# Kernel optimization log

Hardware: AMD Instinct MI355X
Metric: run time of the kernel (lower is better)

Reference implementation:

```python
import jax, jax.numpy as jnp
import numpy as np

N, DIN, DOUT = 8192, 128, 128
NEG = -9.0e15  # the module's -9000000000000000.0 mask value
ALPHA = 0.2    # LeakyReLU negative slope


def setup_inputs() -> dict:
    key = jax.random.key(0)
    kx, ka, kw, ks, kr = jax.random.split(key, 5)
    X = jax.random.normal(kx, (N, DIN), dtype=jnp.float32)
    A = (jax.random.uniform(ka, (N, N)) < 0.01).astype(jnp.float32)
    A = A.at[jnp.arange(N), jnp.arange(N)].set(1.0)
    # Linear weight (Kaiming-uniform-ish range is irrelevant to math; use Xavier)
    lim_w = float(np.sqrt(6.0 / (DIN + DOUT)))
    W = jax.random.uniform(kw, (DOUT, DIN), jnp.float32, -lim_w, lim_w)
    b = jnp.zeros((DOUT,), jnp.float32)
    lim_a = float(np.sqrt(6.0 / (DOUT + 1)))
    a_s = jax.random.uniform(ks, (DOUT, 1), jnp.float32, -lim_a, lim_a)
    a_r = jax.random.uniform(kr, (DOUT, 1), jnp.float32, -lim_a, lim_a)
    return {"X": X, "A": A, "W": W, "b": b, "a_s": a_s, "a_r": a_r}


def reference(X, A, W, b, a_s, a_r):
    # H_in = Linear(X)
    H = X @ W.T + b                         # [N, DOUT]
    s = H @ a_s                             # [N, 1] source scores
    r = H @ a_r                             # [N, 1] receiver scores
    # M_s = A * s (broadcast over cols), M_r = A * r^T (broadcast over rows)
    e = jax.nn.leaky_relu(A * s + A * r.T, negative_slope=ALPHA)  # [N, N]
    masked = jnp.where(A > 0, e, NEG)
    att = jax.nn.softmax(masked, axis=1)    # row-stochastic attention
    H_out = att @ H                         # [N, DOUT]  (act = Identity, dropout = eval)
    # NOTE: the torch module applies LayerNorm into a local var but returns
    # the pre-norm H_out, so LayerNorm is dead code. A and [] passthroughs omitted.
    return H_out
```

## Files before the change

### kernel.cpp

```cpp
#include <hip/hip_runtime.h>

#define N 8192
#define D 128
#define ALPHA 0.2f
#define CAP 1536

__global__ __launch_bounds__(256) void linear_kernel(
    const float* __restrict__ X, const float* __restrict__ W,
    const float* __restrict__ b, const float* __restrict__ a_s,
    const float* __restrict__ a_r,
    float* __restrict__ H, float* __restrict__ sv, float* __restrict__ rv)
{
    __shared__ float Xs[128 * 36];
    __shared__ float Ws[64 * 132];

    const int tid = threadIdx.x;
    const int i0  = blockIdx.x * 32;

    for (int idx = tid; idx < 32 * 128; idx += 256) {
        const int row = idx >> 7, k = idx & 127;
        Xs[k * 36 + row] = X[(i0 + row) * D + k];
    }

    float acc[4][4] = {};
    const int ty = tid >> 5, tx = tid & 31;
    const int rbase = ty * 4, cbase = tx * 4;

    for (int kb = 0; kb < 2; ++kb) {
        __syncthreads();
        for (int idx = tid; idx < 64 * 128; idx += 256) {
            const int o = idx >> 6, kk = idx & 63;
            Ws[kk * 132 + o] = W[o * D + kb * 64 + kk];
        }
        __syncthreads();
        #pragma unroll
        for (int kk = 0; kk < 64; ++kk) {
            const float4 xv = *(const float4*)&Xs[(kb * 64 + kk) * 36 + rbase];
            const float4 wv = *(const float4*)&Ws[kk * 132 + cbase];
            const float xr[4] = {xv.x, xv.y, xv.z, xv.w};
            const float wc[4] = {wv.x, wv.y, wv.z, wv.w};
            #pragma unroll
            for (int r = 0; r < 4; ++r)
                #pragma unroll
                for (int c = 0; c < 4; ++c)
                    acc[r][c] += xr[r] * wc[c];
        }
    }

    const float4 bv  = *(const float4*)&b[cbase];
    const float4 asv = *(const float4*)&a_s[cbase];
    const float4 arv = *(const float4*)&a_r[cbase];
    #pragma unroll
    for (int r = 0; r < 4; ++r) {
        float4 h;
        h.x = acc[r][0] + bv.x;
        h.y = acc[r][1] + bv.y;
        h.z = acc[r][2] + bv.z;
        h.w = acc[r][3] + bv.w;
        *(float4*)&H[(size_t)(i0 + rbase + r) * D + cbase] = h;
        float ps = h.x * asv.x + h.y * asv.y + h.z * asv.z + h.w * asv.w;
        float pr = h.x * arv.x + h.y * arv.y + h.z * arv.z + h.w * arv.w;
        #pragma unroll
        for (int off = 16; off > 0; off >>= 1) {
            ps += __shfl_xor(ps, off);
            pr += __shfl_xor(pr, off);
        }
        if (tx == 0) {
            sv[i0 + rbase + r] = ps;
            rv[i0 + rbase + r] = pr;
        }
    }
}

__global__ __launch_bounds__(256) void attn_kernel(
    const float* __restrict__ A, const float* __restrict__ H,
    const float* __restrict__ sv, const float* __restrict__ rv,
    float* __restrict__ out)
{
    __shared__ int   s_idx[CAP];
    __shared__ float s_z[CAP];
    __shared__ int   s_cnt;
    __shared__ float s_redm[4];
    __shared__ float s_reds[4];
    __shared__ float s_hbuf[128];

    const int tid = threadIdx.x;
    const int i   = blockIdx.x;
    if (tid == 0) s_cnt = 0;
    __syncthreads();

    const float  si   = sv[i];
    const float4* Arow = (const float4*)(A + (size_t)i * N);

    float lm = -3.0e38f;
    #pragma unroll
    for (int it = 0; it < 8; ++it) {
        const int idx4 = it * 256 + tid;
        const float4 a = Arow[idx4];
        const float av[4] = {a.x, a.y, a.z, a.w};
        #pragma unroll
        for (int e = 0; e < 4; ++e) {
            if (av[e] != 0.0f) {
                const int j = idx4 * 4 + e;
                float z = si + rv[j];
                z = (z > 0.0f) ? z : ALPHA * z;
                const int p = atomicAdd(&s_cnt, 1);
                if (p < CAP) { s_idx[p] = j; s_z[p] = z; }
                lm = fmaxf(lm, z);
            }
        }
    }

    #pragma unroll
    for (int off = 32; off > 0; off >>= 1) lm = fmaxf(lm, __shfl_xor(lm, off));
    if ((tid & 63) == 0) s_redm[tid >> 6] = lm;
    __syncthreads();
    const int   cnt = (s_cnt < CAP) ? s_cnt : CAP;
    const float m   = fmaxf(fmaxf(s_redm[0], s_redm[1]), fmaxf(s_redm[2], s_redm[3]));

    float sl = 0.0f;
    for (int p = tid; p < cnt; p += 256) {
        const float w = __expf(s_z[p] - m);
        s_z[p] = w;
        sl += w;
    }
    #pragma unroll
    for (int off = 32; off > 0; off >>= 1) sl += __shfl_xor(sl, off);
    if ((tid & 63) == 0) s_reds[tid >> 6] = sl;
    __syncthreads();
    const float inv = 1.0f / (s_reds[0] + s_reds[1] + s_reds[2] + s_reds[3]);

    const int d = tid & 127, half = tid >> 7;
    float acc = 0.0f;
    for (int p = half; p < cnt; p += 2)
        acc += s_z[p] * H[(size_t)s_idx[p] * D + d];

    if (half == 1) s_hbuf[d] = acc;
    __syncthreads();
    if (half == 0) out[(size_t)i * D + d] = (acc + s_hbuf[d]) * inv;
}

extern "C" void kernel_launch(void* const* d_in, const int* in_sizes, int n_in,
                              void* d_out, int out_size, void* d_ws, size_t ws_size,
                              hipStream_t stream) {
    const float* X   = (const float*)d_in[0];
    const float* A   = (const float*)d_in[1];
    const float* W   = (const float*)d_in[2];
    const float* b   = (const float*)d_in[3];
    const float* a_s = (const float*)d_in[4];
    const float* a_r = (const float*)d_in[5];
    float* out = (float*)d_out;

    float* H  = (float*)d_ws;
    float* sv = H + (size_t)N * D;
    float* rv = sv + N;

    linear_kernel<<<256, 256, 0, stream>>>(X, W, b, a_s, a_r, H, sv, rv);
    attn_kernel<<<N, 256, 0, stream>>>(A, H, sv, rv, out);
}
```

Measured before the change: 445.7 us.

## Split attention into global sparse-list scan and wave-per-row gather kernels

Replaces the per-row block that scanned A with shared-memory atomics by a grid-stride scan kernel. That kernel builds per-row neighbor lists in global memory using wave ballots and aggregated atomics. A separate gather kernel then handles each row with one wave, computing the softmax in registers and accumulating H rows as float2. The aim is better memory-level parallelism on the dense A read and cheaper aggregation, at the cost of an extra memset and launch, a per-row cap of 256 neighbors, and a nondeterministic neighbor order.

```diff
diff --git a/kernel.cpp b/kernel.cpp
--- a/kernel.cpp
+++ b/kernel.cpp
@@ -3,7 +3,7 @@
 #define N 8192
 #define D 128
 #define ALPHA 0.2f
-#define CAP 1536
+#define RCAP 256
 
 __global__ __launch_bounds__(256) void linear_kernel(
     const float* __restrict__ X, const float* __restrict__ W,
@@ -72,72 +72,102 @@
     }
 }
 
-__global__ __launch_bounds__(256) void attn_kernel(
-    const float* __restrict__ A, const float* __restrict__ H,
-    const float* __restrict__ sv, const float* __restrict__ rv,
-    float* __restrict__ out)
+__global__ __launch_bounds__(256) void scan_kernel(
+    const float* __restrict__ A, int* __restrict__ cnt, int* __restrict__ lists)
 {
-    __shared__ int   s_idx[CAP];
-    __shared__ float s_z[CAP];
-    __shared__ int   s_cnt;
-    __shared__ float s_redm[4];
-    __shared__ float s_reds[4];
-    __shared__ float s_hbuf[128];
+    const int lane = threadIdx.x & 63;
+    const unsigned long long lt_mask = (lane == 63) ? 0xFFFFFFFFFFFFFFFFull >> 1
+                                                    : (1ull << lane) - 1;
+    int idx = blockIdx.x * 256 + threadIdx.x;
+    const int stride = gridDim.x * 256;
+    const float4* __restrict__ A4 = (const float4*)A;
 
-    const int tid = threadIdx.x;
-    const int i   = blockIdx.x;
-    if (tid == 0) s_cnt = 0;
-    __syncthreads();
+    #pragma unroll 1
+    for (int it = 0; it < 32; ++it, idx += stride) {
+        const float4 a = A4[idx];
+        const int row  = idx >> 11;
+        const int col0 = (idx & 2047) * 4;
+        const float av[4] = {a.x, a.y, a.z, a.w};
+        #pragma unroll
+        for (int e = 0; e < 4; ++e) {
+            const bool nz = (av[e] != 0.0f);
+            const unsigned long long mask = __ballot(nz);
+            if (mask == 0ull) continue;
+            const int leader = __ffsll((long long)mask) - 1;
+            int base = 0;
+            if (lane == leader) base = atomicAdd(&cnt[row], __popcll(mask));
+            base = __shfl(base, leader);
+            if (nz) {
+                const int off = __popcll(mask & lt_mask);
+                const int p = base + off;
+                if (p < RCAP) lists[row * RCAP + p] = col0 + e;
+            }
+        }
+    }
+}
 
-    const float  si   = sv[i];
-    const float4* Arow = (const float4*)(A + (size_t)i * N);
+__global__ __launch_bounds__(256) void gather_kernel(
+    const float* __restrict__ H, const float* __restrict__ sv,
+    const float* __restrict__ rv, const int* __restrict__ cnt,
+    const int* __restrict__ lists, float* __restrict__ out)
+{
+    __shared__ float s_w[4][RCAP];
+    __shared__ int   s_j[4][RCAP];
+
+    const int wave = threadIdx.x >> 6;
+    const int lane = threadIdx.x & 63;
+    const int i = blockIdx.x * 4 + wave;
+
+    int c = cnt[i];
+    c = (c < RCAP) ? c : RCAP;
+    const float si = sv[i];
+
+    float zv[4];
+    int   jv[4];
+    int kn = 0;
+    for (int p = lane; p < c; p += 64, ++kn) {
+        const int j = lists[i * RCAP + p];
+        float z = si + rv[j];
+        z = (z > 0.0f) ? z : ALPHA * z;
+        jv[kn] = j;
+        zv[kn] = z;
+    }
 
     float lm = -3.0e38f;
     #pragma unroll
-    for (int it = 0; it < 8; ++it) {
-        const int idx4 = it * 256 + tid;
-        const float4 a = Arow[idx4];
-        const float av[4] = {a.x, a.y, a.z, a.w};
-        #pragma unroll
-        for (int e = 0; e < 4; ++e) {
-            if (av[e] != 0.0f) {
-                const int j = idx4 * 4 + e;
-                float z = si + rv[j];
-                z = (z > 0.0f) ? z : ALPHA * z;
-                const int p = atomicAdd(&s_cnt, 1);
-                if (p < CAP) { s_idx[p] = j; s_z[p] = z; }
-                lm = fmaxf(lm, z);
-            }
+    for (int k = 0; k < 4; ++k) if (k < kn) lm = fmaxf(lm, zv[k]);
+    #pragma unroll
+    for (int off = 32; off > 0; off >>= 1) lm = fmaxf(lm, __shfl_xor(lm, off));
+
+    float sl = 0.0f;
+    #pragma unroll
+    for (int k = 0; k < 4; ++k) if (k < kn) { zv[k] = __expf(zv[k] - lm); sl += zv[k]; }
+    #pragma unroll
+    for (int off = 32; off > 0; off >>= 1) sl += __shfl_xor(sl, off);
+    const float inv = 1.0f / sl;
+
+    {
+        int k = 0;
+        for (int p = lane; p < c; p += 64, ++k) {
+            s_w[wave][p] = zv[k];
+            s_j[wave][p] = jv[k];
         }
     }
+    __syncthreads();
 
-    #pragma unroll
-    for (int off = 32; off > 0; off >>= 1) lm = fmaxf(lm, __shfl_xor(lm, off));
-    if ((tid & 63) == 0) s_redm[tid >> 6] = lm;
-    __syncthreads();
-    const int   cnt = (s_cnt < CAP) ? s_cnt : CAP;
-    const float m   = fmaxf(fmaxf(s_redm[0], s_redm[1]), fmaxf(s_redm[2], s_redm[3]));
-
-    float sl = 0.0f;
-    for (int p = tid; p < cnt; p += 256) {
-        const float w = __expf(s_z[p] - m);
-        s_z[p] = w;
-        sl += w;
+    float2 acc = make_float2(0.0f, 0.0f);
+    const float* __restrict__ Hl = H + 2 * lane;
+    #pragma unroll 4
+    for (int p = 0; p < c; ++p) {
+        const float w = s_w[wave][p];
+        const int   j = s_j[wave][p];
+        const float2 h = *(const float2*)&Hl[(size_t)j * D];
+        acc.x += w * h.x;
+        acc.y += w * h.y;
     }
-    #pragma unroll
-    for (int off = 32; off > 0; off >>= 1) sl += __shfl_xor(sl, off);
-    if ((tid & 63) == 0) s_reds[tid >> 6] = sl;
-    __syncthreads();
-    const float inv = 1.0f / (s_reds[0] + s_reds[1] + s_reds[2] + s_reds[3]);
-
-    const int d = tid & 127, half = tid >> 7;
-    float acc = 0.0f;
-    for (int p = half; p < cnt; p += 2)
-        acc += s_z[p] * H[(size_t)s_idx[p] * D + d];
-
-    if (half == 1) s_hbuf[d] = acc;
-    __syncthreads();
-    if (half == 0) out[(size_t)i * D + d] = (acc + s_hbuf[d]) * inv;
+    acc.x *= inv;
+    acc.y *= inv;
+    *(float2*)&out[(size_t)i * D + 2 * lane] = acc;
 }
 
 extern "C" void kernel_launch(void* const* d_in, const int* in_sizes, int n_in,
@@ -151,10 +181,14 @@
     const float* a_r = (const float*)d_in[5];
     float* out = (float*)d_out;
 
-    float* H  = (float*)d_ws;
-    float* sv = H + (size_t)N * D;
-    float* rv = sv + N;
+    float* H   = (float*)d_ws;
+    float* sv  = H + (size_t)N * D;
+    float* rv  = sv + N;
+    int*   cnt = (int*)(rv + N);
+    int*   lists = cnt + N;
 
+    hipMemsetAsync(cnt, 0, N * sizeof(int), stream);
     linear_kernel<<<256, 256, 0, stream>>>(X, W, b, a_s, a_r, H, sv, rv);
-    attn_kernel<<<N, 256, 0, stream>>>(A, H, sv, rv, out);
+    scan_kernel<<<2048, 256, 0, stream>>>(A, cnt, lists);
+    gather_kernel<<<2048, 256, 0, stream>>>(H, sv, rv, cnt, lists, out);
 }
```

Result: no change. 452.9 us (+1.6%).

## Process one attention row per wavefront with ballot-based neighbor compaction

Applied to the files above, without the earlier changes.

The attention kernel now assigns one row per 64-lane wavefront (four rows per block), so it no longer needs block-wide barriers or shared-memory reductions. Nonzero columns are compacted with ballot/popcount prefix sums instead of shared atomics, and the loads of A are software-prefetched one step ahead. Softmax runs in registers, and aggregation has each lane accumulate two output columns through float2 loads of H. The risk is the neighbor cap, now 256 per row (about 82 expected per row), which silently truncates unusually dense rows. There is also less memory-level parallelism per row while streaming A.

```diff
diff --git a/kernel.cpp b/kernel.cpp
--- a/kernel.cpp
+++ b/kernel.cpp
@@ -3,7 +3,7 @@
 #define N 8192
 #define D 128
 #define ALPHA 0.2f
-#define CAP 1536
+#define RCAP 256
 
 __global__ __launch_bounds__(256) void linear_kernel(
     const float* __restrict__ X, const float* __restrict__ W,
@@ -72,72 +72,87 @@
     }
 }
 
-__global__ __launch_bounds__(256) void attn_kernel(
+__global__ __launch_bounds__(256, 8) void attn_fused(
     const float* __restrict__ A, const float* __restrict__ H,
     const float* __restrict__ sv, const float* __restrict__ rv,
     float* __restrict__ out)
 {
-    __shared__ int   s_idx[CAP];
-    __shared__ float s_z[CAP];
-    __shared__ int   s_cnt;
-    __shared__ float s_redm[4];
-    __shared__ float s_reds[4];
-    __shared__ float s_hbuf[128];
+    __shared__ float2 s_l[4][RCAP];
 
-    const int tid = threadIdx.x;
-    const int i   = blockIdx.x;
-    if (tid == 0) s_cnt = 0;
-    __syncthreads();
+    const int wave = threadIdx.x >> 6;
+    const int lane = threadIdx.x & 63;
+    const int i    = blockIdx.x * 4 + wave;
+    const unsigned long long lt = (1ull << lane) - 1ull;
 
-    const float  si   = sv[i];
-    const float4* Arow = (const float4*)(A + (size_t)i * N);
+    const float4* __restrict__ Arow = (const float4*)(A + (size_t)i * N);
 
-    float lm = -3.0e38f;
-    #pragma unroll
-    for (int it = 0; it < 8; ++it) {
-        const int idx4 = it * 256 + tid;
-        const float4 a = Arow[idx4];
-        const float av[4] = {a.x, a.y, a.z, a.w};
+    int cnt = 0;
+    float4 cur = Arow[lane];
+    #pragma unroll 1
+    for (int it = 0; it < 32; ++it) {
+        float4 nxt = make_float4(0.f, 0.f, 0.f, 0.f);
+        if (it < 31) nxt = Arow[(it + 1) * 64 + lane];
+        const int col0 = it * 256 + lane * 4;
+        const float av[4] = {cur.x, cur.y, cur.z, cur.w};
         #pragma unroll
         for (int e = 0; e < 4; ++e) {
-            if (av[e] != 0.0f) {
-                const int j = idx4 * 4 + e;
-                float z = si + rv[j];
-                z = (z > 0.0f) ? z : ALPHA * z;
-                const int p = atomicAdd(&s_cnt, 1);
-                if (p < CAP) { s_idx[p] = j; s_z[p] = z; }
-                lm = fmaxf(lm, z);
+            const bool nz = (av[e] != 0.0f);
+            const unsigned long long m = __ballot(nz);
+            if (nz) {
+                const int pos = cnt + __popcll(m & lt);
+                if (pos < RCAP) s_l[wave][pos].y = __int_as_float(col0 + e);
             }
+            cnt += __popcll(m);
         }
+        cur = nxt;
     }
+    cnt = (cnt < RCAP) ? cnt : RCAP;
 
+    const float si = sv[i];
+    float zv[4];
+    #pragma unroll
+    for (int k = 0; k < 4; ++k) {
+        const int p = lane + 64 * k;
+        const bool act = (p < cnt);
+        const int j = act ? __float_as_int(s_l[wave][p].y) : 0;
+        float z = si + rv[j];
+        z = (z > 0.0f) ? z : ALPHA * z;
+        zv[k] = act ? z : -3.0e38f;
+    }
+    float lm = fmaxf(fmaxf(zv[0], zv[1]), fmaxf(zv[2], zv[3]));
     #pragma unroll
     for (int off = 32; off > 0; off >>= 1) lm = fmaxf(lm, __shfl_xor(lm, off));
-    if ((tid & 63) == 0) s_redm[tid >> 6] = lm;
-    __syncthreads();
-    const int   cnt = (s_cnt < CAP) ? s_cnt : CAP;
-    const float m   = fmaxf(fmaxf(s_redm[0], s_redm[1]), fmaxf(s_redm[2], s_redm[3]));
 
     float sl = 0.0f;
-    for (int p = tid; p < cnt; p += 256) {
-        const float w = __expf(s_z[p] - m);
-        s_z[p] = w;
+    float wv4[4];
+    #pragma unroll
+    for (int k = 0; k < 4; ++k) {
+        const int p = lane + 64 * k;
+        const float w = (p < cnt) ? __expf(zv[k] - lm) : 0.0f;
+        wv4[k] = w;
         sl += w;
     }
     #pragma unroll
     for (int off = 32; off > 0; off >>= 1) sl += __shfl_xor(sl, off);
-    if ((tid & 63) == 0) s_reds[tid >> 6] = sl;
-    __syncthreads();
-    const float inv = 1.0f / (s_reds[0] + s_reds[1] + s_reds[2] + s_reds[3]);
+    const float inv = 1.0f / sl;
 
-    const int d = tid & 127, half = tid >> 7;
-    float acc = 0.0f;
-    for (int p = half; p < cnt; p += 2)
-        acc += s_z[p] * H[(size_t)s_idx[p] * D + d];
+    #pragma unroll
+    for (int k = 0; k < 4; ++k) {
+        const int p = lane + 64 * k;
+        if (p < cnt) s_l[wave][p].x = wv4[k] * inv;
+    }
 
-    if (half == 1) s_hbuf[d] = acc;
-    __syncthreads();
-    if (half == 0) out[(size_t)i * D + d] = (acc + s_hbuf[d]) * inv;
+    float2 acc = make_float2(0.0f, 0.0f);
+    const float* __restrict__ Hl = H + 2 * lane;
+    #pragma unroll 4
+    for (int p = 0; p < cnt; ++p) {
+        const float2 wj = s_l[wave][p];
+        const int   j  = __float_as_int(wj.y);
+        const float2 h = *(const float2*)&Hl[(size_t)j * D];
+        acc.x += wj.x * h.x;
+        acc.y += wj.x * h.y;
+    }
+    *(float2*)&out[(size_t)i * D + 2 * lane] = acc;
 }
 
 extern "C" void kernel_launch(void* const* d_in, const int* in_sizes, int n_in,
@@ -156,5 +171,5 @@
     float* rv = sv + N;
 
     linear_kernel<<<256, 256, 0, stream>>>(X, W, b, a_s, a_r, H, sv, rv);
-    attn_kernel<<<N, 256, 0, stream>>>(A, H, sv, rv, out);
+    attn_fused<<<N / 4, 256, 0, stream>>>(A, H, sv, rv, out);
 }
```

Result: faster. 402.4 us (-9.7%).
